# Kernel tuning notes

Measured on AMD Instinct MI355X. Metric: run time of the kernel, lower is better.

## Reference

```python
import jax, jax.numpy as jnp
import numpy as np

S, B, E, H, D, P = 4096, 8, 1024, 16, 64, 64


def setup_inputs() -> dict:
    key = jax.random.key(0)
    ks = jax.random.split(key, 6)
    scale = 1.0 / np.sqrt(E)
    return {
        "x": jax.random.normal(ks[0], (S, B, E), dtype=jnp.float32),
        "w_qkv": jax.random.normal(ks[1], (3 * E, E), dtype=jnp.float32) * scale,
        "w_out": jax.random.normal(ks[2], (E, E), dtype=jnp.float32) * scale,
        "b_out": jax.random.normal(ks[3], (E,), dtype=jnp.float32) * 0.01,
        "w_f": jax.random.normal(ks[4], (P, D), dtype=jnp.float32) * (1.0 / np.sqrt(D)),
        "b_f": jax.random.normal(ks[5], (P,), dtype=jnp.float32) * 0.01,
    }


def reference(x, w_qkv, w_out, b_out, w_f, b_f):
    # x: (S, B, E). qkv_proj has no bias.
    qkv = jnp.einsum("sbe,fe->sbf", x, w_qkv)  # (S, B, 3E)
    q, k, v = jnp.split(qkv, 3, axis=-1)

    def to_heads(t):
        # view (S,B,H,D) then transpose(0,2) -> (H,B,S,D)
        return t.reshape(S, B, H, D).transpose(2, 1, 0, 3)

    q, k, v = to_heads(q), to_heads(k), to_heads(v)

    # feature map: Linear(D->P) + ReLU, applied to q and k
    q_p = jax.nn.relu(jnp.einsum("hbsd,pd->hbsp", q, w_f) + b_f)
    k_p = jax.nn.relu(jnp.einsum("hbsd,pd->hbsp", k, w_f) + b_f)

    # linear attention: O(n) via k'^T v then q' @ (k'^T v)
    kv = jnp.einsum("hbsp,hbsd->hbpd", k_p, v)          # (H,B,P,D)
    num = jnp.einsum("hbsp,hbpd->hbsd", q_p, kv)         # (H,B,S,D)
    k_sum = k_p.sum(axis=-2)                              # (H,B,P)
    normalizer = jnp.einsum("hbsp,hbp->hbs", q_p, k_sum)[..., None]  # (H,B,S,1)
    attn = num / (normalizer + 1e-8)

    # back to (S, B, E)
    out = attn.transpose(2, 1, 0, 3).reshape(S, B, E)
    return jnp.einsum("sbe,fe->sbf", out, w_out) + b_out
```

## Files before the change

### kernel.cpp

```cpp
#include <hip/hip_runtime.h>
#include <hip/hip_bf16.h>
#include <stdint.h>

#define S_LEN 4096
#define B_DIM 8
#define E_DIM 1024
#define H_DIM 16
#define M_ROWS (S_LEN * B_DIM)
#define N_QKV (3 * E_DIM)
#define HB_DIM (H_DIM * B_DIM)

typedef float f32x4 __attribute__((ext_vector_type(4)));
typedef short bf16x8 __attribute__((ext_vector_type(8)));

#define MFMA16(a, b, c) __builtin_amdgcn_mfma_f32_16x16x32_bf16(a, b, c, 0, 0, 0)

__device__ __forceinline__ short f2bf(float f) {
  __hip_bfloat16 h = __float2bfloat16(f);
  short s;
  __builtin_memcpy(&s, &h, 2);
  return s;
}
__device__ __forceinline__ float bf2f(short b) {
  unsigned u = ((unsigned)(unsigned short)b) << 16;
  float f;
  __builtin_memcpy(&f, &u, 4);
  return f;
}
__device__ __forceinline__ void gl_lds16(const void* g, void* l) {
  __builtin_amdgcn_global_load_lds(
      (const __attribute__((address_space(1))) void*)g,
      (__attribute__((address_space(3))) void*)l, 16, 0, 0);
}

__global__ __launch_bounds__(256) void cast_all(
    const float* __restrict__ x, const float* __restrict__ wqkv,
    const float* __restrict__ wout, const float* __restrict__ wf,
    short* __restrict__ xb, short* __restrict__ wqb,
    short* __restrict__ wob, short* __restrict__ wfb) {
  const long n_x = (long)M_ROWS * E_DIM;
  const long n_wq = 3L * E_DIM * E_DIM;
  const long n_wo = (long)E_DIM * E_DIM;
  long idx = ((long)blockIdx.x * 256 + threadIdx.x) * 4;
  const float* src;
  short* dst;
  if (idx < n_x) {
    src = x + idx; dst = xb + idx;
  } else if ((idx -= n_x) < n_wq) {
    src = wqkv + idx; dst = wqb + idx;
  } else if ((idx -= n_wq) < n_wo) {
    src = wout + idx; dst = wob + idx;
  } else {
    idx -= n_wo;
    src = wf + idx; dst = wfb + idx;
  }
  float4 v = *(const float4*)src;
  short4 o;
  o.x = f2bf(v.x); o.y = f2bf(v.y); o.z = f2bf(v.z); o.w = f2bf(v.w);
  *(short4*)dst = o;
}

__device__ __forceinline__ void mma16q(f32x4 acc[8][4], const bf16x8 afr[2][2],
                                       const bf16x8 bfr[4][2], int m0) {
#pragma unroll
  for (int kk = 0; kk < 2; kk++)
#pragma unroll
    for (int ii = 0; ii < 2; ii++)
#pragma unroll
      for (int ni = 0; ni < 4; ni++)
        acc[m0 + ii][ni] = MFMA16(afr[ii][kk], bfr[ni][kk], acc[m0 + ii][ni]);
}

template <int OUT_F32>
__global__ __launch_bounds__(512, 2) void gemm256(
    const short* __restrict__ A, const short* __restrict__ Bm,
    void* __restrict__ Cout, const float* __restrict__ bias, int N, int K) {
  __shared__ short L[65536];
  char* Lb = (char*)L;
  const int t = threadIdx.x;
  const int w = t >> 6, l = t & 63;
  const int q = l >> 4, c = l & 15;
  const int wm = w >> 2, wn = w & 3;

  const int nwg = gridDim.x;
  const int cpx = nwg >> 3;
  const int lid = ((int)blockIdx.x & 7) * cpx + ((int)blockIdx.x >> 3);
  const int bm = (lid & 127) << 8;
  const int bn = (lid >> 7) << 8;

  const long Kb = (long)K * 2;
  const int srow = t >> 3;
  const int scb = (((t & 7) ^ ((t >> 3) & 7)) << 4);
  const char* gA = (const char*)A + (long)(bm + srow) * Kb + scb;
  const char* gB = (const char*)Bm + (long)(bn + srow) * Kb + scb;
  const long r64 = 64 * Kb;

#define STAGE_A(h, srcT, dbuf)                                      \
  do {                                                              \
    const char* s_ = gA + (long)(srcT) * 128 + (long)(h) * 2 * r64; \
    char* d_ = Lb + (dbuf) * 32768 + (h) * 16384 + (w << 10);       \
    gl_lds16(s_, d_);                                               \
    gl_lds16(s_ + r64, d_ + 8192);                                  \
  } while (0)
#define STAGE_B(h, srcT, dbuf)                                      \
  do {                                                              \
    const char* s_ = gB + (long)(srcT) * 128 + (long)(h) * 2 * r64; \
    char* d_ = Lb + 65536 + (dbuf) * 32768 + (h) * 16384 + (w << 10); \
    gl_lds16(s_, d_);                                               \
    gl_lds16(s_ + r64, d_ + 8192);                                  \
  } while (0)

  const int sw = c & 7;
  const int s0 = (q ^ sw) << 3;
  const int s1 = s0 ^ 32;
  const int aoff = wm * 8192 + c * 64;
  const int boff = 32768 + (wn >> 1) * 8192 + ((wn & 1) * 64 + c) * 64;

#define LDA(dst, mi, kk) \
  dst = *(const bf16x8*)(L + bufo + aoff + (mi) * 1024 + ((kk) ? s1 : s0))
#define LDB(dst, ni, kk) \
  dst = *(const bf16x8*)(L + bufo + boff + (ni) * 1024 + ((kk) ? s1 : s0))

  f32x4 acc[8][4];
#pragma unroll
  for (int i = 0; i < 8; i++)
#pragma unroll
    for (int j = 0; j < 4; j++) acc[i][j] = (f32x4){0.f, 0.f, 0.f, 0.f};

  const int NT = K >> 6;

  STAGE_A(0, 0, 0);
  STAGE_A(1, 0, 0);
  STAGE_B(0, 0, 0);
  STAGE_B(1, 0, 0);
  STAGE_B(0, 1, 1);
  STAGE_B(1, 1, 1);
  asm volatile("s_waitcnt vmcnt(4)\n\ts_barrier" ::: "memory");

  for (int T = 0; T < NT; ++T) {
    const int bufo = (T & 1) * 16384;
    const int TA = (T + 1 < NT) ? T + 1 : NT - 1;
    const int TB = (T + 2 < NT) ? T + 2 : NT - 1;
    const int bufA = (T + 1) & 1;
    const int bufB = T & 1;

    bf16x8 bfr[4][2], afr[2][2];

#pragma unroll
    for (int ni = 0; ni < 4; ni++) {
      LDB(bfr[ni][0], ni, 0);
      LDB(bfr[ni][1], ni, 1);
    }
    LDA(afr[0][0], 0, 0); LDA(afr[0][1], 0, 1);
    LDA(afr[1][0], 1, 0); LDA(afr[1][1], 1, 1);
    STAGE_A(0, TA, bufA);
    __builtin_amdgcn_s_barrier();
    __builtin_amdgcn_s_setprio(1);
    mma16q(acc, afr, bfr, 0);
    __builtin_amdgcn_s_setprio(0);
    __builtin_amdgcn_s_barrier();

    LDA(afr[0][0], 2, 0); LDA(afr[0][1], 2, 1);
    LDA(afr[1][0], 3, 0); LDA(afr[1][1], 3, 1);
    STAGE_A(1, TA, bufA);
    __builtin_amdgcn_s_barrier();
    __builtin_amdgcn_s_setprio(1);
    mma16q(acc, afr, bfr, 2);
    __builtin_amdgcn_s_setprio(0);
    __builtin_amdgcn_s_barrier();

    LDA(afr[0][0], 4, 0); LDA(afr[0][1], 4, 1);
    LDA(afr[1][0], 5, 0); LDA(afr[1][1], 5, 1);
    STAGE_B(0, TB, bufB);
    __builtin_amdgcn_s_barrier();
    __builtin_amdgcn_s_setprio(1);
    mma16q(acc, afr, bfr, 4);
    __builtin_amdgcn_s_setprio(0);
    __builtin_amdgcn_s_barrier();

    LDA(afr[0][0], 6, 0); LDA(afr[0][1], 6, 1);
    LDA(afr[1][0], 7, 0); LDA(afr[1][1], 7, 1);
    STAGE_B(1, TB, bufB);
    __builtin_amdgcn_s_barrier();
    __builtin_amdgcn_s_setprio(1);
    mma16q(acc, afr, bfr, 6);
    __builtin_amdgcn_s_setprio(0);
    asm volatile("s_waitcnt vmcnt(4)\n\ts_barrier" ::: "memory");
  }
  asm volatile("s_waitcnt vmcnt(0)" ::: "memory");

#undef STAGE_A
#undef STAGE_B
#undef LDA
#undef LDB

  if (OUT_F32) {
    float* C = (float*)Cout;
#pragma unroll
    for (int ni = 0; ni < 4; ni++) {
      int n = bn + (wn << 6) + ni * 16 + c;
      float bo = bias[n];
#pragma unroll
      for (int mi = 0; mi < 8; mi++)
#pragma unroll
        for (int r = 0; r < 4; r++) {
          int m = bm + (wm << 7) + mi * 16 + (q << 2) + r;
          C[(long)m * N + n] = acc[mi][ni][r] + bo;
        }
    }
  } else {
    short* C = (short*)Cout;
#pragma unroll
    for (int ni = 0; ni < 4; ni++) {
      int n = bn + (wn << 6) + ni * 16 + c;
#pragma unroll
      for (int mi = 0; mi < 8; mi++)
#pragma unroll
        for (int r = 0; r < 4; r++) {
          int m = bm + (wm << 7) + mi * 16 + (q << 2) + r;
          C[(long)m * N + n] = f2bf(acc[mi][ni][r]);
        }
    }
  }
}

__global__ __launch_bounds__(256) void feature_kernel(
    const short* __restrict__ qkv, const short* __restrict__ wfb,
    const float* __restrict__ b_f, short* __restrict__ Qp,
    short* __restrict__ KpT, short* __restrict__ VT) {
  const int bx = blockIdx.x;
  const int sblk = bx & 15, b = (bx >> 4) & 7, h = bx >> 7;
  const int t = threadIdx.x, w = t >> 6, l = t & 63;
  const int q = l >> 4, c = l & 15;
  const int s_base = sblk * 256 + w * 64;
  const int hb = h * 8 + b;

  bf16x8 wf[4][2];
#pragma unroll
  for (int ti = 0; ti < 4; ti++)
#pragma unroll
    for (int kk = 0; kk < 2; kk++)
      wf[ti][kk] = *(const bf16x8*)(wfb + (ti * 16 + c) * 64 + kk * 32 + q * 8);

  float bfc[4];
#pragma unroll
  for (int ni = 0; ni < 4; ni++) bfc[ni] = b_f[ni * 16 + c];

  f32x4 acc[4][4];
  bf16x8 xf[4][2];

#pragma unroll
  for (int i = 0; i < 4; i++)
#pragma unroll
    for (int j = 0; j < 4; j++) acc[i][j] = (f32x4){0.f, 0.f, 0.f, 0.f};
#pragma unroll
  for (int mi = 0; mi < 4; mi++) {
    long ridx = (long)((s_base + mi * 16 + c) * 8 + b) * N_QKV;
#pragma unroll
    for (int kk = 0; kk < 2; kk++)
      xf[mi][kk] = *(const bf16x8*)(qkv + ridx + h * 64 + kk * 32 + q * 8);
  }
#pragma unroll
  for (int kk = 0; kk < 2; kk++)
#pragma unroll
    for (int mi = 0; mi < 4; mi++)
#pragma unroll
      for (int ni = 0; ni < 4; ni++)
        acc[mi][ni] = MFMA16(xf[mi][kk], wf[ni][kk], acc[mi][ni]);
#pragma unroll
  for (int mi = 0; mi < 4; mi++)
#pragma unroll
    for (int ni = 0; ni < 4; ni++)
#pragma unroll
      for (int r = 0; r < 4; r++) {
        int s = s_base + mi * 16 + q * 4 + r;
        float v = acc[mi][ni][r] + bfc[ni];
        v = fmaxf(v, 0.f);
        Qp[((long)hb * S_LEN + s) * 64 + ni * 16 + c] = f2bf(v);
      }

#pragma unroll
  for (int i = 0; i < 4; i++)
#pragma unroll
    for (int j = 0; j < 4; j++) acc[i][j] = (f32x4){0.f, 0.f, 0.f, 0.f};
#pragma unroll
  for (int si = 0; si < 4; si++) {
    long ridx = (long)((s_base + si * 16 + c) * 8 + b) * N_QKV;
#pragma unroll
    for (int kk = 0; kk < 2; kk++)
      xf[si][kk] =
          *(const bf16x8*)(qkv + ridx + E_DIM + h * 64 + kk * 32 + q * 8);
  }
#pragma unroll
  for (int kk = 0; kk < 2; kk++)
#pragma unroll
    for (int pi = 0; pi < 4; pi++)
#pragma unroll
      for (int si = 0; si < 4; si++)
        acc[pi][si] = MFMA16(wf[pi][kk], xf[si][kk], acc[pi][si]);
#pragma unroll
  for (int pi = 0; pi < 4; pi++)
#pragma unroll
    for (int r = 0; r < 4; r++) {
      int p = pi * 16 + q * 4 + r;
      float bb = b_f[p];
#pragma unroll
      for (int si = 0; si < 4; si++) {
        int s = s_base + si * 16 + c;
        float v = acc[pi][si][r] + bb;
        v = fmaxf(v, 0.f);
        KpT[((long)hb * 64 + p) * S_LEN + s] = f2bf(v);
      }
    }

  bf16x8 id0 = {0, 0, 0, 0, 0, 0, 0, 0}, id1 = {0, 0, 0, 0, 0, 0, 0, 0};
#pragma unroll
  for (int j = 0; j < 8; j++) {
    int k = q * 8 + j;
    id0[j] = (short)((k == c) ? 0x3F80 : 0);
    id1[j] = (short)((k == c + 16) ? 0x3F80 : 0);
  }
#pragma unroll
  for (int i = 0; i < 4; i++)
#pragma unroll
    for (int j = 0; j < 4; j++) acc[i][j] = (f32x4){0.f, 0.f, 0.f, 0.f};
#pragma unroll
  for (int si = 0; si < 4; si++) {
    long ridx = (long)((s_base + si * 16 + c) * 8 + b) * N_QKV;
#pragma unroll
    for (int kc = 0; kc < 2; kc++)
      xf[si][kc] =
          *(const bf16x8*)(qkv + ridx + 2 * E_DIM + h * 64 + kc * 32 + q * 8);
  }
#pragma unroll
  for (int kc = 0; kc < 2; kc++)
#pragma unroll
    for (int si = 0; si < 4; si++) {
      acc[kc * 2 + 0][si] = MFMA16(id0, xf[si][kc], acc[kc * 2 + 0][si]);
      acc[kc * 2 + 1][si] = MFMA16(id1, xf[si][kc], acc[kc * 2 + 1][si]);
    }
#pragma unroll
  for (int dt = 0; dt < 4; dt++)
#pragma unroll
    for (int si = 0; si < 4; si++)
#pragma unroll
      for (int r = 0; r < 4; r++) {
        int d = (dt >> 1) * 32 + (dt & 1) * 16 + q * 4 + r;
        int s = s_base + si * 16 + c;
        VT[((long)hb * 64 + d) * S_LEN + s] = f2bf(acc[dt][si][r]);
      }
}

__global__ __launch_bounds__(256) void kv_kernel(const short* __restrict__ KpT,
                                                 const short* __restrict__ VT,
                                                 float* __restrict__ kvf) {
  const int hb = blockIdx.y, sc = blockIdx.x;
  const int t = threadIdx.x, w = t >> 6, l = t & 63;
  const int q = l >> 4, c = l & 15;
  const int s0 = sc * 512 + w * 128;
  const short* vb = VT + (long)hb * 64 * S_LEN;
  const short* kb = KpT + (long)hb * 64 * S_LEN;

  f32x4 acc[4][4];
#pragma unroll
  for (int i = 0; i < 4; i++)
#pragma unroll
    for (int j = 0; j < 4; j++) acc[i][j] = (f32x4){0.f, 0.f, 0.f, 0.f};

  for (int it = 0; it < 4; it++) {
    int so = s0 + it * 32 + q * 8;
    bf16x8 af[4], bfr[4];
#pragma unroll
    for (int di = 0; di < 4; di++)
      af[di] = *(const bf16x8*)(vb + (long)(di * 16 + c) * S_LEN + so);
#pragma unroll
    for (int pi = 0; pi < 4; pi++)
      bfr[pi] = *(const bf16x8*)(kb + (long)(pi * 16 + c) * S_LEN + so);
#pragma unroll
    for (int di = 0; di < 4; di++)
#pragma unroll
      for (int pi = 0; pi < 4; pi++)
        acc[di][pi] = MFMA16(af[di], bfr[pi], acc[di][pi]);
  }

  __shared__ float red[4][4096];
#pragma unroll
  for (int di = 0; di < 4; di++)
#pragma unroll
    for (int pi = 0; pi < 4; pi++)
#pragma unroll
      for (int r = 0; r < 4; r++)
        red[w][(di * 16 + q * 4 + r) * 64 + pi * 16 + c] = acc[di][pi][r];
  __syncthreads();
  float* dst = kvf + (long)hb * 4096;
  for (int i = 0; i < 16; i++) {
    int idx = i * 256 + t;
    float s = red[0][idx] + red[1][idx] + red[2][idx] + red[3][idx];
    atomicAdd(dst + idx, s);
  }
}

__global__ __launch_bounds__(256) void kv_cast(const float* __restrict__ kvf,
                                               short* __restrict__ kvb) {
  int i = blockIdx.x * 256 + threadIdx.x;
  kvb[i] = f2bf(kvf[i]);
}

__global__ __launch_bounds__(256) void ksum_kernel(const short* __restrict__ KpT,
                                                   short* __restrict__ ksum) {
  const int hb = blockIdx.x;
  const int t = threadIdx.x, w = t >> 6, l = t & 63;
  for (int pi = 0; pi < 16; pi++) {
    int p = w * 16 + pi;
    const short* row = KpT + ((long)hb * 64 + p) * S_LEN;
    float s = 0.f;
#pragma unroll
    for (int i = 0; i < 8; i++) {
      bf16x8 v = *(const bf16x8*)(row + i * 512 + l * 8);
#pragma unroll
      for (int j = 0; j < 8; j++) s += bf2f(v[j]);
    }
    for (int off = 32; off > 0; off >>= 1) s += __shfl_down(s, off, 64);
    if (l == 0) ksum[hb * 64 + p] = f2bf(s);
  }
}

__global__ __launch_bounds__(256) void attn_kernel(
    const short* __restrict__ Qp, const short* __restrict__ kvb,
    const short* __restrict__ ksum, short* __restrict__ attn) {
  const int bx = blockIdx.x;
  const int sblk = bx & 15, b = (bx >> 4) & 7, h = bx >> 7;
  const int t = threadIdx.x, w = t >> 6, l = t & 63;
  const int q = l >> 4, c = l & 15;
  const int s_base = sblk * 256 + w * 64;
  const int hb = h * 8 + b;

  bf16x8 bkv[4][2];
#pragma unroll
  for (int ni = 0; ni < 4; ni++)
#pragma unroll
    for (int kk = 0; kk < 2; kk++)
      bkv[ni][kk] = *(const bf16x8*)(kvb + (long)hb * 4096 +
                                     (ni * 16 + c) * 64 + kk * 32 + q * 8);
  bf16x8 bn[2];
  const bf16x8 zfrag = {0, 0, 0, 0, 0, 0, 0, 0};
#pragma unroll
  for (int kk = 0; kk < 2; kk++) {
    bf16x8 v = *(const bf16x8*)(ksum + hb * 64 + kk * 32 + q * 8);
    bn[kk] = (c == 0) ? v : zfrag;
  }

  bf16x8 af[4][2];
#pragma unroll
  for (int mi = 0; mi < 4; mi++)
#pragma unroll
    for (int kk = 0; kk < 2; kk++)
      af[mi][kk] = *(const bf16x8*)(Qp + ((long)hb * S_LEN + s_base + mi * 16 + c) * 64 +
                                    kk * 32 + q * 8);

  f32x4 acc[4][4], accn[4];
#pragma unroll
  for (int i = 0; i < 4; i++) {
    accn[i] = (f32x4){0.f, 0.f, 0.f, 0.f};
#pragma unroll
    for (int j = 0; j < 4; j++) acc[i][j] = (f32x4){0.f, 0.f, 0.f, 0.f};
  }
#pragma unroll
  for (int kk = 0; kk < 2; kk++)
#pragma unroll
    for (int mi = 0; mi < 4; mi++) {
      accn[mi] = MFMA16(af[mi][kk], bn[kk], accn[mi]);
#pragma unroll
      for (int ni = 0; ni < 4; ni++)
        acc[mi][ni] = MFMA16(af[mi][kk], bkv[ni][kk], acc[mi][ni]);
    }

#pragma unroll
  for (int mi = 0; mi < 4; mi++)
#pragma unroll
    for (int r = 0; r < 4; r++) {
      float nv = __shfl(accn[mi][r], l & 48, 64);
      float inv = 1.f / (nv + 1e-8f);
      int s = s_base + mi * 16 + q * 4 + r;
#pragma unroll
      for (int ni = 0; ni < 4; ni++) {
        float v = acc[mi][ni][r] * inv;
        attn[((long)s * 8 + b) * E_DIM + h * 64 + ni * 16 + c] = f2bf(v);
      }
    }
}

extern "C" void kernel_launch(void* const* d_in, const int* in_sizes, int n_in,
                              void* d_out, int out_size, void* d_ws,
                              size_t ws_size, hipStream_t stream) {
  const float* x = (const float*)d_in[0];
  const float* w_qkv = (const float*)d_in[1];
  const float* w_out = (const float*)d_in[2];
  const float* b_out = (const float*)d_in[3];
  const float* w_f = (const float*)d_in[4];
  const float* b_f = (const float*)d_in[5];

  char* ws = (char*)d_ws;
  constexpr size_t off_xb = 0;
  constexpr size_t off_wqb = 67108864;
  constexpr size_t off_wob = off_wqb + 6291456;
  constexpr size_t off_wfb = off_wob + 2097152;
  constexpr size_t off_qkv = off_wfb + 8192;
  constexpr size_t off_Qp = off_qkv + 201326592;
  constexpr size_t off_KpT = off_Qp + 67108864;
  constexpr size_t off_VT = off_KpT + 67108864;
  constexpr size_t off_kvf = off_VT + 67108864;
  constexpr size_t off_kvb = off_kvf + 2097152;
  constexpr size_t off_ksum = off_kvb + 1048576;

  short* xb = (short*)(ws + off_xb);
  short* wqb = (short*)(ws + off_wqb);
  short* wob = (short*)(ws + off_wob);
  short* wfb = (short*)(ws + off_wfb);
  short* qkv = (short*)(ws + off_qkv);
  short* Qp = (short*)(ws + off_Qp);
  short* KpT = (short*)(ws + off_KpT);
  short* VT = (short*)(ws + off_VT);
  float* kvf = (float*)(ws + off_kvf);
  short* kvb = (short*)(ws + off_kvb);
  short* ksum = (short*)(ws + off_ksum);
  short* attn = xb;

  cast_all<<<36868, 256, 0, stream>>>(x, w_qkv, w_out, w_f, xb, wqb, wob, wfb);

  gemm256<0><<<1536, 512, 0, stream>>>(xb, wqb, qkv, nullptr, N_QKV, E_DIM);

  feature_kernel<<<2048, 256, 0, stream>>>(qkv, wfb, b_f, Qp, KpT, VT);

  hipMemsetAsync(kvf, 0, (size_t)HB_DIM * 4096 * 4, stream);
  kv_kernel<<<dim3(8, HB_DIM), 256, 0, stream>>>(KpT, VT, kvf);
  kv_cast<<<2048, 256, 0, stream>>>(kvf, kvb);
  ksum_kernel<<<HB_DIM, 256, 0, stream>>>(KpT, ksum);

  attn_kernel<<<2048, 256, 0, stream>>>(Qp, kvb, ksum, attn);

  gemm256<1><<<512, 512, 0, stream>>>(attn, wob, (float*)d_out, b_out,
                                      E_DIM, E_DIM);
}
```

Before: 736.4 us.

## Fold k-sum into kv MFMA kernel and remap GEMM block swizzle

Removes the separate ksum kernel: the k-feature column sums are now computed inside kv_kernel with an extra MFMA against an all-ones bf16 fragment and accumulated atomically into a float buffer. That buffer reuses the qkv workspace, which is dead by then, and its bf16 cast is folded into the kv_cast launch. This drops one launch and a second full read of KpT. The GEMM block-to-tile mapping also changes: each group of blocks now covers 16 consecutive M tiles within a band, which alters L2 locality.

```diff
diff --git a/kernel.cpp b/kernel.cpp
--- a/kernel.cpp
+++ b/kernel.cpp
@@ -82,11 +82,10 @@
   const int q = l >> 4, c = l & 15;
   const int wm = w >> 2, wn = w & 3;
 
-  const int nwg = gridDim.x;
-  const int cpx = nwg >> 3;
-  const int lid = ((int)blockIdx.x & 7) * cpx + ((int)blockIdx.x >> 3);
-  const int bm = (lid & 127) << 8;
-  const int bn = (lid >> 7) << 8;
+  const int band = (int)blockIdx.x & 7;
+  const int i = (int)blockIdx.x >> 3;
+  const int bm = ((band << 4) + (i & 15)) << 8;
+  const int bn = (i >> 4) << 8;
 
   const long Kb = (long)K * 2;
   const int srow = t >> 3;
@@ -123,9 +122,9 @@
 
   f32x4 acc[8][4];
 #pragma unroll
-  for (int i = 0; i < 8; i++)
-#pragma unroll
-    for (int j = 0; j < 4; j++) acc[i][j] = (f32x4){0.f, 0.f, 0.f, 0.f};
+  for (int ii = 0; ii < 8; ii++)
+#pragma unroll
+    for (int j = 0; j < 4; j++) acc[ii][j] = (f32x4){0.f, 0.f, 0.f, 0.f};
 
   const int NT = K >> 6;
 
@@ -353,7 +352,8 @@
 
 __global__ __launch_bounds__(256) void kv_kernel(const short* __restrict__ KpT,
                                                  const short* __restrict__ VT,
-                                                 float* __restrict__ kvf) {
+                                                 float* __restrict__ kvf,
+                                                 float* __restrict__ ksumf) {
   const int hb = blockIdx.y, sc = blockIdx.x;
   const int t = threadIdx.x, w = t >> 6, l = t & 63;
   const int q = l >> 4, c = l & 15;
@@ -361,11 +361,17 @@
   const short* vb = VT + (long)hb * 64 * S_LEN;
   const short* kb = KpT + (long)hb * 64 * S_LEN;
 
-  f32x4 acc[4][4];
-#pragma unroll
-  for (int i = 0; i < 4; i++)
+  bf16x8 ones;
+#pragma unroll
+  for (int j = 0; j < 8; j++) ones[j] = (short)0x3F80;
+
+  f32x4 acc[4][4], acc5[4];
+#pragma unroll
+  for (int i = 0; i < 4; i++) {
+    acc5[i] = (f32x4){0.f, 0.f, 0.f, 0.f};
 #pragma unroll
     for (int j = 0; j < 4; j++) acc[i][j] = (f32x4){0.f, 0.f, 0.f, 0.f};
+  }
 
   for (int it = 0; it < 4; it++) {
     int so = s0 + it * 32 + q * 8;
@@ -381,6 +387,9 @@
 #pragma unroll
       for (int pi = 0; pi < 4; pi++)
         acc[di][pi] = MFMA16(af[di], bfr[pi], acc[di][pi]);
+#pragma unroll
+    for (int pi = 0; pi < 4; pi++)
+      acc5[pi] = MFMA16(ones, bfr[pi], acc5[pi]);
   }
 
   __shared__ float red[4][4096];
@@ -398,30 +407,23 @@
     float s = red[0][idx] + red[1][idx] + red[2][idx] + red[3][idx];
     atomicAdd(dst + idx, s);
   }
+  if (q == 0) {
+#pragma unroll
+    for (int pi = 0; pi < 4; pi++)
+      atomicAdd(ksumf + hb * 64 + pi * 16 + c, acc5[pi][0]);
+  }
 }
 
 __global__ __launch_bounds__(256) void kv_cast(const float* __restrict__ kvf,
-                                               short* __restrict__ kvb) {
+                                               short* __restrict__ kvb,
+                                               const float* __restrict__ ksumf,
+                                               short* __restrict__ ksum) {
   int i = blockIdx.x * 256 + threadIdx.x;
-  kvb[i] = f2bf(kvf[i]);
-}
-
-__global__ __launch_bounds__(256) void ksum_kernel(const short* __restrict__ KpT,
-                                                   short* __restrict__ ksum) {
-  const int hb = blockIdx.x;
-  const int t = threadIdx.x, w = t >> 6, l = t & 63;
-  for (int pi = 0; pi < 16; pi++) {
-    int p = w * 16 + pi;
-    const short* row = KpT + ((long)hb * 64 + p) * S_LEN;
-    float s = 0.f;
-#pragma unroll
-    for (int i = 0; i < 8; i++) {
-      bf16x8 v = *(const bf16x8*)(row + i * 512 + l * 8);
-#pragma unroll
-      for (int j = 0; j < 8; j++) s += bf2f(v[j]);
-    }
-    for (int off = 32; off > 0; off >>= 1) s += __shfl_down(s, off, 64);
-    if (l == 0) ksum[hb * 64 + p] = f2bf(s);
+  if (i < 524288) {
+    kvb[i] = f2bf(kvf[i]);
+  } else if (i < 524288 + 8192) {
+    int j = i - 524288;
+    ksum[j] = f2bf(ksumf[j]);
   }
 }
 
@@ -524,6 +526,7 @@
   float* kvf = (float*)(ws + off_kvf);
   short* kvb = (short*)(ws + off_kvb);
   short* ksum = (short*)(ws + off_ksum);
+  float* ksumf = (float*)(ws + off_qkv);
   short* attn = xb;
 
   cast_all<<<36868, 256, 0, stream>>>(x, w_qkv, w_out, w_f, xb, wqb, wob, wfb);
@@ -533,9 +536,9 @@
   feature_kernel<<<2048, 256, 0, stream>>>(qkv, wfb, b_f, Qp, KpT, VT);
 
   hipMemsetAsync(kvf, 0, (size_t)HB_DIM * 4096 * 4, stream);
-  kv_kernel<<<dim3(8, HB_DIM), 256, 0, stream>>>(KpT, VT, kvf);
-  kv_cast<<<2048, 256, 0, stream>>>(kvf, kvb);
-  ksum_kernel<<<HB_DIM, 256, 0, stream>>>(KpT, ksum);
+  hipMemsetAsync(ksumf, 0, (size_t)HB_DIM * 64 * 4, stream);
+  kv_kernel<<<dim3(8, HB_DIM), 256, 0, stream>>>(KpT, VT, kvf, ksumf);
+  kv_cast<<<2080, 256, 0, stream>>>(kvf, kvb, ksumf, ksum);
 
   attn_kernel<<<2048, 256, 0, stream>>>(Qp, kvb, ksum, attn);
 
```

Result: faster. 720.4 us (-2.2%).
